# Optimization experiments

Hardware: AMD Instinct MI355X
Metric: run time of the kernel (lower is better)

The kernel has to match this reference:

```python
import jax, jax.numpy as jnp
import numpy as np

T, D, H = 2048, 256, 256
DISCOUNT = 0.99
LAMBDA = 0.9
CONT_ALPHA = 0.01


def setup_inputs() -> dict:
    key = jax.random.key(0)
    ks = jax.random.split(key, 5)
    xs = jax.random.normal(ks[0], (T, D), jnp.float32)
    gs = jax.random.normal(ks[1], (T,), jnp.float32)            # returns / targets
    dones = (jax.random.uniform(ks[2], (T,)) < 0.02).astype(jnp.float32)  # sparse episode ends
    ys = jnp.stack([gs, dones], axis=1)                          # [T, 2] as in train_step
    W1 = jax.random.normal(ks[3], (D, H), jnp.float32) * (1.0 / float(np.sqrt(D)))
    b1 = jnp.zeros((H,), jnp.float32)
    W2 = jax.random.normal(ks[4], (H, 1), jnp.float32) * (1.0 / float(np.sqrt(H)))
    b2 = jnp.zeros((1,), jnp.float32)
    return {"xs": xs, "ys": ys, "W1": W1, "b1": b1, "W2": W2, "b2": b2}


def _value(params, x):
    # Value network: self(x)[0] for a batch of 1 -> scalar prediction.
    W1, b1, W2, b2 = params
    h = jax.nn.relu(x @ W1 + b1)          # [H]
    return (h @ W2 + b2)[0]               # scalar us


def _td_lambda(xs, ys, W1, b1, W2, b2):
    params = (W1, b1, W2, b2)
    gs, dones = ys[:, 0], ys[:, 1]
    zeros = tuple(jnp.zeros_like(p) for p in params)
    val_grad = jax.value_and_grad(_value)

    def step(carry, inp):
        z, total, r = carry
        x, g, done = inp
        us, grads = val_grad(params, x)   # grads of the PREDICTION us, as in tape.gradient(us, vars)
        error = (g - us) ** 2             # compiled_loss (MSE) on a single sample
        sigma = error - r                 # continuing TD error
        r = r + CONT_ALPHA * sigma
        # eligibility trace update and accumulated update
        z = tuple(DISCOUNT * LAMBDA * zi + gi for zi, gi in zip(z, grads))
        total = tuple(ti - sigma * zi for ti, zi in zip(total, z))
        # episode reset: zero traces and average-reward estimate when done
        keep = 1.0 - (done > 0.5).astype(jnp.float32)
        z = tuple(zi * keep for zi in z)
        r = r * keep
        return (z, total, r), sigma

    init = (zeros, zeros, jnp.float32(0.0))
    (_, total, _), sigmas = jax.lax.scan(step, init, (xs, gs, dones))
    # accumulated gradients for all trainable vars (flattened) + final sigma (reported loss)
    return jnp.concatenate([t.ravel() for t in total] + [sigmas[-1][None]])


def reference(xs, ys, W1, b1, W2, b2):
    return _td_lambda(xs, ys, W1, b1, W2, b2)
```

## Files before the change

kernel.cpp:

```cpp
#include <hip/hip_runtime.h>

#define GL  0.891f
#define OMA 0.99f
#define AL  0.01f

#define OFF_H   0
#define OFF_U   524288
#define OFF_PW1 526336
#define OFF_PB1 788480
#define OFF_PW2 789504
#define WS_FLOATS 790528

__global__ __launch_bounds__(1024, 4) void fwd_kernel(
    const float* __restrict__ xs, const float* __restrict__ W1,
    const float* __restrict__ b1, const float* __restrict__ W2,
    const float* __restrict__ b2,
    float* __restrict__ Hbuf, float* __restrict__ u) {
  const int tid = threadIdx.x;
  const int j2 = tid & 127;
  const int kq = tid >> 7;
  const int kb = kq * 32;
  const int r0 = blockIdx.x * 8;
  __shared__ __align__(16) float xsl[8 * 260];
  __shared__ __align__(16) float part[8 * 2048];

  if (tid < 512) {
    const int row = tid >> 6;
    const int q4 = tid & 63;
    *reinterpret_cast<float4*>(&xsl[row * 260 + 4 * q4]) =
        *reinterpret_cast<const float4*>(&xs[(r0 + row) * 256 + 4 * q4]);
  }

  float wcur[16], wnxt[16];
#pragma unroll
  for (int kk = 0; kk < 8; ++kk) {
    wcur[2 * kk + 0] = W1[(kb + kk) * 256 + j2];
    wcur[2 * kk + 1] = W1[(kb + kk) * 256 + j2 + 128];
  }
  __syncthreads();

  float acc[16];
#pragma unroll
  for (int m = 0; m < 16; ++m) acc[m] = 0.f;
#pragma unroll
  for (int b = 0; b < 4; ++b) {
    if (b < 3) {
#pragma unroll
      for (int kk = 0; kk < 8; ++kk) {
        wnxt[2 * kk + 0] = W1[(kb + (b + 1) * 8 + kk) * 256 + j2];
        wnxt[2 * kk + 1] = W1[(kb + (b + 1) * 8 + kk) * 256 + j2 + 128];
      }
    }
    const int k = kb + b * 8;
#pragma unroll
    for (int r = 0; r < 8; ++r) {
      const float4 x0 = *reinterpret_cast<const float4*>(&xsl[r * 260 + k]);
      const float4 x1 = *reinterpret_cast<const float4*>(&xsl[r * 260 + k + 4]);
      float a0 = acc[r * 2 + 0], a1 = acc[r * 2 + 1];
      a0 = fmaf(x0.x, wcur[0], a0);  a1 = fmaf(x0.x, wcur[1], a1);
      a0 = fmaf(x0.y, wcur[2], a0);  a1 = fmaf(x0.y, wcur[3], a1);
      a0 = fmaf(x0.z, wcur[4], a0);  a1 = fmaf(x0.z, wcur[5], a1);
      a0 = fmaf(x0.w, wcur[6], a0);  a1 = fmaf(x0.w, wcur[7], a1);
      a0 = fmaf(x1.x, wcur[8], a0);  a1 = fmaf(x1.x, wcur[9], a1);
      a0 = fmaf(x1.y, wcur[10], a0); a1 = fmaf(x1.y, wcur[11], a1);
      a0 = fmaf(x1.z, wcur[12], a0); a1 = fmaf(x1.z, wcur[13], a1);
      a0 = fmaf(x1.w, wcur[14], a0); a1 = fmaf(x1.w, wcur[15], a1);
      acc[r * 2 + 0] = a0; acc[r * 2 + 1] = a1;
    }
#pragma unroll
    for (int m = 0; m < 16; ++m) wcur[m] = wnxt[m];
  }

#pragma unroll
  for (int r = 0; r < 8; ++r) {
    part[kq * 2048 + r * 256 + j2] = acc[r * 2 + 0];
    part[kq * 2048 + r * 256 + j2 + 128] = acc[r * 2 + 1];
  }
  __syncthreads();
#pragma unroll
  for (int q = 0; q < 2; ++q) {
    const int s = tid + q * 1024;
    const int j = s & 255;
    float a = b1[j];
#pragma unroll
    for (int kk = 0; kk < 8; ++kk) a += part[kk * 2048 + s];
    const float h = fmaxf(a, 0.f);
    Hbuf[r0 * 256 + s] = h;
    part[s] = h * W2[j];
  }
  __syncthreads();
  {
    const int r = tid >> 7;
    const int jj = tid & 127;
    part[r * 256 + jj] += part[r * 256 + jj + 128];
    __syncthreads();
    if (jj < 64) {
      float v = part[r * 256 + jj] + part[r * 256 + jj + 64];
#pragma unroll
      for (int s = 32; s >= 1; s >>= 1) v += __shfl_xor(v, s, 64);
      if (jj == 0) u[r0 + r] = v + b2[0];
    }
  }
}

__global__ __launch_bounds__(512, 4) void scan_w1_kernel(
    const float* __restrict__ u, const float* __restrict__ ys,
    const float* __restrict__ xs, const float* __restrict__ Hbuf,
    const float* __restrict__ W2,
    float* __restrict__ pW1, float* __restrict__ pB1, float* __restrict__ pW2,
    float* __restrict__ outp) {
  const int tid = threadIdx.x;
  const int blk = blockIdx.x;
  const int tq = blk & 3;
  const int tile = blk >> 2;
  const int dcb = tile >> 3;
  const int jc = tile & 7;
  const int d0 = dcb * 16;
  const int j0 = jc * 32;
  const int tb = tq * 512;
  const int lane = tid & 63;
  const int w = tid >> 6;
  const int jq = lane & 7;
  const int dh = (lane >> 3) & 3;
  const int tt2 = lane >> 5;
  const int tloc = w * 64 + tt2 * 32;
  const int jcol = j0 + 4 * jq;

  __shared__ __align__(16) float xt[512 * 20];
  __shared__ __align__(16) float c_l[512];
  __shared__ __align__(16) float red[8 * 576];
  __shared__ float aggA[8], aggB[8], ag2A[8], ag2B[8], wsum[8];

  const float* Hp = Hbuf + jcol;
  float4 hc[8], hn[8];
#pragma unroll
  for (int i = 0; i < 8; ++i)
    hc[i] = *reinterpret_cast<const float4*>(Hp + (tb + tloc + i) * 256);

#pragma unroll
  for (int q = 0; q < 4; ++q) {
    const int idx = tid + q * 512;
    const int row = idx >> 2;
    const int qd = idx & 3;
    *reinterpret_cast<float4*>(&xt[row * 20 + 4 * qd]) =
        *reinterpret_cast<const float4*>(&xs[(tb + row) * 256 + d0 + 4 * qd]);
  }

  float e[4], kp[4];
  {
    const float4 u4 = ((const float4*)u)[tid];
    const float uu[4] = {u4.x, u4.y, u4.z, u4.w};
#pragma unroll
    for (int q = 0; q < 2; ++q) {
      const float4 y = ((const float4*)ys)[2 * tid + q];
      const float da = y.x - uu[2 * q];
      const float db = y.z - uu[2 * q + 1];
      e[2 * q] = da * da;
      e[2 * q + 1] = db * db;
      kp[2 * q] = (y.y > 0.5f) ? 0.f : 1.f;
      kp[2 * q + 1] = (y.w > 0.5f) ? 0.f : 1.f;
    }
  }
  float A = 1.f, B = 0.f;
#pragma unroll
  for (int i = 0; i < 4; ++i) {
    const float a = kp[i] * OMA;
    B = fmaf(a, B, kp[i] * (AL * e[i]));
    A *= a;
  }
#pragma unroll
  for (int s = 1; s < 64; s <<= 1) {
    const float pA = __shfl_up(A, s, 64);
    const float pB = __shfl_up(B, s, 64);
    if (lane >= s) { B = fmaf(A, pB, B); A *= pA; }
  }
  if (lane == 63) { aggA[w] = A; aggB[w] = B; }
  __syncthreads();
  float rin;
  {
    float rw = 0.f;
    for (int v = 0; v < w; ++v) rw = fmaf(aggA[v], rw, aggB[v]);
    float lA = __shfl_up(A, 1, 64);
    float lB = __shfl_up(B, 1, 64);
    if (lane == 0) { lA = 1.f; lB = 0.f; }
    rin = fmaf(lA, rw, lB);
  }
  float sig[4];
  {
    float r = rin;
#pragma unroll
    for (int i = 0; i < 4; ++i) {
      sig[i] = e[i] - r;
      const float a = kp[i] * OMA;
      r = fmaf(a, r, kp[i] * (AL * e[i]));
    }
  }
  if (blk == 0 && tid == 511) outp[66049] = sig[3];

  float A2 = 1.f, B2 = 0.f;
#pragma unroll
  for (int i = 3; i >= 0; --i) {
    const float a = GL * kp[i];
    B2 = fmaf(a, B2, -sig[i]);
    A2 *= a;
  }
#pragma unroll
  for (int s = 1; s < 64; s <<= 1) {
    const float nA = __shfl_down(A2, s, 64);
    const float nB = __shfl_down(B2, s, 64);
    if (lane + s < 64) { B2 = fmaf(A2, nB, B2); A2 *= nA; }
  }
  if (lane == 0) { ag2A[w] = A2; ag2B[w] = B2; }
  __syncthreads();
  float cin;
  {
    float cw = 0.f;
    for (int v = 7; v > w; --v) cw = fmaf(ag2A[v], cw, ag2B[v]);
    float lA = __shfl_down(A2, 1, 64);
    float lB = __shfl_down(B2, 1, 64);
    if (lane == 63) { lA = 1.f; lB = 0.f; }
    cin = fmaf(lA, cw, lB);
  }
  float cr[4];
  float cc = cin, csum = 0.f;
#pragma unroll
  for (int i = 3; i >= 0; --i) {
    cc = fmaf(GL * kp[i], cc, -sig[i]);
    cr[i] = cc;
    csum += cc;
  }
  if ((tid >> 7) == tq) {
    const int bl = 4 * (tid - tq * 128);
    *reinterpret_cast<float4*>(&c_l[bl]) = make_float4(cr[0], cr[1], cr[2], cr[3]);
  }
  if (blk == 0) {
#pragma unroll
    for (int s = 32; s >= 1; s >>= 1) csum += __shfl_xor(csum, s, 64);
    if (lane == 0) wsum[w] = csum;
  }
  __syncthreads();
  if (blk == 0 && tid == 0) {
    float s = 0.f;
#pragma unroll
    for (int v = 0; v < 8; ++v) s += wsum[v];
    outp[66048] = s;
  }

  const float4 w24 = *reinterpret_cast<const float4*>(W2 + jcol);
  float acc[16];
#pragma unroll
  for (int m = 0; m < 16; ++m) acc[m] = 0.f;
  float sb[4] = {0.f, 0.f, 0.f, 0.f}, sw[4] = {0.f, 0.f, 0.f, 0.f};
  const bool do_bw = (dcb == 0);

#pragma unroll
  for (int b = 0; b < 4; ++b) {
    if (b < 3) {
#pragma unroll
      for (int i = 0; i < 8; ++i)
        hn[i] = *reinterpret_cast<const float4*>(
            Hp + (tb + tloc + (b + 1) * 8 + i) * 256);
    }
#pragma unroll
    for (int i = 0; i < 8; ++i) {
      const int row = tloc + b * 8 + i;
      const float ct = c_l[row];
      const float4 h = hc[i];
      const float gc0 = (h.x > 0.f) ? w24.x * ct : 0.f;
      const float gc1 = (h.y > 0.f) ? w24.y * ct : 0.f;
      const float gc2 = (h.z > 0.f) ? w24.z * ct : 0.f;
      const float gc3 = (h.w > 0.f) ? w24.w * ct : 0.f;
      if (do_bw) {
        sb[0] += gc0; sb[1] += gc1; sb[2] += gc2; sb[3] += gc3;
        sw[0] = fmaf(ct, h.x, sw[0]); sw[1] = fmaf(ct, h.y, sw[1]);
        sw[2] = fmaf(ct, h.z, sw[2]); sw[3] = fmaf(ct, h.w, sw[3]);
      }
      const float4 xv = *reinterpret_cast<const float4*>(&xt[row * 20 + dh * 4]);
      acc[0]  = fmaf(gc0, xv.x, acc[0]);
      acc[1]  = fmaf(gc1, xv.x, acc[1]);
      acc[2]  = fmaf(gc2, xv.x, acc[2]);
      acc[3]  = fmaf(gc3, xv.x, acc[3]);
      acc[4]  = fmaf(gc0, xv.y, acc[4]);
      acc[5]  = fmaf(gc1, xv.y, acc[5]);
      acc[6]  = fmaf(gc2, xv.y, acc[6]);
      acc[7]  = fmaf(gc3, xv.y, acc[7]);
      acc[8]  = fmaf(gc0, xv.z, acc[8]);
      acc[9]  = fmaf(gc1, xv.z, acc[9]);
      acc[10] = fmaf(gc2, xv.z, acc[10]);
      acc[11] = fmaf(gc3, xv.z, acc[11]);
      acc[12] = fmaf(gc0, xv.w, acc[12]);
      acc[13] = fmaf(gc1, xv.w, acc[13]);
      acc[14] = fmaf(gc2, xv.w, acc[14]);
      acc[15] = fmaf(gc3, xv.w, acc[15]);
    }
#pragma unroll
    for (int i = 0; i < 8; ++i) hc[i] = hn[i];
  }

#pragma unroll
  for (int m = 0; m < 16; ++m) acc[m] += __shfl_xor(acc[m], 32, 64);
  if (do_bw) {
#pragma unroll
    for (int c = 0; c < 4; ++c) {
      sb[c] += __shfl_xor(sb[c], 8, 64);
      sb[c] += __shfl_xor(sb[c], 16, 64);
      sb[c] += __shfl_xor(sb[c], 32, 64);
      sw[c] += __shfl_xor(sw[c], 8, 64);
      sw[c] += __shfl_xor(sw[c], 16, 64);
      sw[c] += __shfl_xor(sw[c], 32, 64);
    }
  }
  if (lane < 32) {
#pragma unroll
    for (int x = 0; x < 4; ++x)
      *reinterpret_cast<float4*>(&red[w * 576 + (dh * 4 + x) * 32 + jq * 4]) =
          make_float4(acc[x * 4 + 0], acc[x * 4 + 1], acc[x * 4 + 2], acc[x * 4 + 3]);
  }
  if (do_bw && lane < 8) {
    *reinterpret_cast<float4*>(&red[w * 576 + 16 * 32 + lane * 4]) =
        make_float4(0.25f * sb[0], 0.25f * sb[1], 0.25f * sb[2], 0.25f * sb[3]);
    *reinterpret_cast<float4*>(&red[w * 576 + 17 * 32 + lane * 4]) =
        make_float4(0.25f * sw[0], 0.25f * sw[1], 0.25f * sw[2], 0.25f * sw[3]);
  }
  __syncthreads();
  {
    const int col = tid & 31;
    const int dd = tid >> 5;
    float s = 0.f;
#pragma unroll
    for (int v = 0; v < 8; ++v) s += red[v * 576 + dd * 32 + col];
    pW1[tq * 65536 + (d0 + dd) * 256 + j0 + col] = s;
  }
  if (do_bw && tid < 64) {
    const int col = tid & 31;
    const int sel = tid >> 5;
    float s = 0.f;
#pragma unroll
    for (int v = 0; v < 8; ++v) s += red[v * 576 + (16 + sel) * 32 + col];
    (sel ? pW2 : pB1)[tq * 256 + j0 + col] = s;
  }
}

__global__ __launch_bounds__(256) void reduce_kernel(
    const float* __restrict__ pW1, const float* __restrict__ pB1,
    const float* __restrict__ pW2, float* __restrict__ outp) {
  if (blockIdx.x < 64) {
    const int i0 = blockIdx.x * 1024 + threadIdx.x * 4;
    float4 s = make_float4(0.f, 0.f, 0.f, 0.f);
#pragma unroll
    for (int q = 0; q < 4; ++q) {
      const float4 v = *reinterpret_cast<const float4*>(pW1 + q * 65536 + i0);
      s.x += v.x; s.y += v.y; s.z += v.z; s.w += v.w;
    }
    *reinterpret_cast<float4*>(outp + i0) = s;
  } else {
    const int j = threadIdx.x;
    float sb = 0.f, sw = 0.f;
#pragma unroll
    for (int q = 0; q < 4; ++q) {
      sb += pB1[q * 256 + j];
      sw += pW2[q * 256 + j];
    }
    outp[65536 + j] = sb;
    outp[65792 + j] = sw;
  }
}

extern "C" void kernel_launch(void* const* d_in, const int* in_sizes, int n_in,
                              void* d_out, int out_size, void* d_ws, size_t ws_size,
                              hipStream_t stream) {
  const float* xs = (const float*)d_in[0];
  const float* ys = (const float*)d_in[1];
  const float* W1 = (const float*)d_in[2];
  const float* b1 = (const float*)d_in[3];
  const float* W2 = (const float*)d_in[4];
  const float* b2 = (const float*)d_in[5];
  float* outp = (float*)d_out;
  float* ws = (float*)d_ws;

  if (ws_size < (size_t)WS_FLOATS * sizeof(float)) return;

  float* Hbuf = ws + OFF_H;
  float* ubuf = ws + OFF_U;
  float* pW1  = ws + OFF_PW1;
  float* pB1  = ws + OFF_PB1;
  float* pW2  = ws + OFF_PW2;

  fwd_kernel<<<256, 1024, 0, stream>>>(xs, W1, b1, W2, b2, Hbuf, ubuf);
  scan_w1_kernel<<<512, 512, 0, stream>>>(ubuf, ys, xs, Hbuf, W2,
                                          pW1, pB1, pW2, outp);
  reduce_kernel<<<65, 256, 0, stream>>>(pW1, pB1, pW2, outp);
}
```

Before: 26.88 us.

## Drop time-split partials and reduce kernel; each block covers all timesteps

The scan/W1-gradient kernel no longer splits the time axis into four quarters that write partial sums reduced by a third kernel. Each block now owns a smaller 8x16 (d,j) tile across all 2048 timesteps and writes final results directly to the output. xs is streamed from global memory into registers with double buffering instead of being staged in shared memory. This removes one kernel launch and the partial-buffer round trip. In exchange each block runs a longer serial loop and does more cross-lane shuffle reductions.

```diff
diff --git a/kernel.cpp b/kernel.cpp
--- a/kernel.cpp
+++ b/kernel.cpp
@@ -4,12 +4,9 @@
 #define OMA 0.99f
 #define AL  0.01f
 
-#define OFF_H   0
-#define OFF_U   524288
-#define OFF_PW1 526336
-#define OFF_PB1 788480
-#define OFF_PW2 789504
-#define WS_FLOATS 790528
+#define OFF_H 0
+#define OFF_U 524288
+#define WS_FLOATS 526336
 
 __global__ __launch_bounds__(1024, 4) void fwd_kernel(
     const float* __restrict__ xs, const float* __restrict__ W1,
@@ -106,44 +103,33 @@
 __global__ __launch_bounds__(512, 4) void scan_w1_kernel(
     const float* __restrict__ u, const float* __restrict__ ys,
     const float* __restrict__ xs, const float* __restrict__ Hbuf,
-    const float* __restrict__ W2,
-    float* __restrict__ pW1, float* __restrict__ pB1, float* __restrict__ pW2,
-    float* __restrict__ outp) {
+    const float* __restrict__ W2, float* __restrict__ outp) {
   const int tid = threadIdx.x;
   const int blk = blockIdx.x;
-  const int tq = blk & 3;
-  const int tile = blk >> 2;
-  const int dcb = tile >> 3;
-  const int jc = tile & 7;
-  const int d0 = dcb * 16;
-  const int j0 = jc * 32;
-  const int tb = tq * 512;
+  const int dcb = blk >> 4;
+  const int jc = blk & 15;
+  const int d0 = dcb * 8;
+  const int j0 = jc * 16;
   const int lane = tid & 63;
   const int w = tid >> 6;
-  const int jq = lane & 7;
-  const int dh = (lane >> 3) & 3;
-  const int tt2 = lane >> 5;
-  const int tloc = w * 64 + tt2 * 32;
+  const int jq = lane & 3;
+  const int dh = (lane >> 2) & 1;
+  const int tt2 = lane >> 3;
+  const int tbase = w * 64 + tt2 * 8;
   const int jcol = j0 + 4 * jq;
-
-  __shared__ __align__(16) float xt[512 * 20];
-  __shared__ __align__(16) float c_l[512];
-  __shared__ __align__(16) float red[8 * 576];
+  const int dcol = d0 + 4 * dh;
+
+  __shared__ __align__(16) float c_l[2048];
+  __shared__ __align__(16) float red[1280];
   __shared__ float aggA[8], aggB[8], ag2A[8], ag2B[8], wsum[8];
 
   const float* Hp = Hbuf + jcol;
-  float4 hc[8], hn[8];
-#pragma unroll
-  for (int i = 0; i < 8; ++i)
-    hc[i] = *reinterpret_cast<const float4*>(Hp + (tb + tloc + i) * 256);
-
-#pragma unroll
-  for (int q = 0; q < 4; ++q) {
-    const int idx = tid + q * 512;
-    const int row = idx >> 2;
-    const int qd = idx & 3;
-    *reinterpret_cast<float4*>(&xt[row * 20 + 4 * qd]) =
-        *reinterpret_cast<const float4*>(&xs[(tb + row) * 256 + d0 + 4 * qd]);
+  const float* Xp = xs + dcol;
+  float4 hc[4], hn[4], xc[4], xn[4];
+#pragma unroll
+  for (int i = 0; i < 4; ++i) {
+    hc[i] = *reinterpret_cast<const float4*>(Hp + (tbase + i) * 256);
+    xc[i] = *reinterpret_cast<const float4*>(Xp + (tbase + i) * 256);
   }
 
   float e[4], kp[4];
@@ -229,10 +215,7 @@
     cr[i] = cc;
     csum += cc;
   }
-  if ((tid >> 7) == tq) {
-    const int bl = 4 * (tid - tq * 128);
-    *reinterpret_cast<float4*>(&c_l[bl]) = make_float4(cr[0], cr[1], cr[2], cr[3]);
-  }
+  *reinterpret_cast<float4*>(&c_l[4 * tid]) = make_float4(cr[0], cr[1], cr[2], cr[3]);
   if (blk == 0) {
 #pragma unroll
     for (int s = 32; s >= 1; s >>= 1) csum += __shfl_xor(csum, s, 64);
@@ -253,19 +236,22 @@
   float sb[4] = {0.f, 0.f, 0.f, 0.f}, sw[4] = {0.f, 0.f, 0.f, 0.f};
   const bool do_bw = (dcb == 0);
 
-#pragma unroll
-  for (int b = 0; b < 4; ++b) {
-    if (b < 3) {
-#pragma unroll
-      for (int i = 0; i < 8; ++i)
-        hn[i] = *reinterpret_cast<const float4*>(
-            Hp + (tb + tloc + (b + 1) * 8 + i) * 256);
-    }
-#pragma unroll
-    for (int i = 0; i < 8; ++i) {
-      const int row = tloc + b * 8 + i;
-      const float ct = c_l[row];
+#pragma unroll 1
+  for (int r8 = 0; r8 < 8; ++r8) {
+    const int tcur = (r8 >> 1) * 512 + tbase + (r8 & 1) * 4;
+    if (r8 < 7) {
+      const int tnx = ((r8 + 1) >> 1) * 512 + tbase + ((r8 + 1) & 1) * 4;
+#pragma unroll
+      for (int i = 0; i < 4; ++i) {
+        hn[i] = *reinterpret_cast<const float4*>(Hp + (tnx + i) * 256);
+        xn[i] = *reinterpret_cast<const float4*>(Xp + (tnx + i) * 256);
+      }
+    }
+#pragma unroll
+    for (int i = 0; i < 4; ++i) {
+      const float ct = c_l[tcur + i];
       const float4 h = hc[i];
+      const float4 xv = xc[i];
       const float gc0 = (h.x > 0.f) ? w24.x * ct : 0.f;
       const float gc1 = (h.y > 0.f) ? w24.y * ct : 0.f;
       const float gc2 = (h.z > 0.f) ? w24.z * ct : 0.f;
@@ -275,7 +261,6 @@
         sw[0] = fmaf(ct, h.x, sw[0]); sw[1] = fmaf(ct, h.y, sw[1]);
         sw[2] = fmaf(ct, h.z, sw[2]); sw[3] = fmaf(ct, h.w, sw[3]);
       }
-      const float4 xv = *reinterpret_cast<const float4*>(&xt[row * 20 + dh * 4]);
       acc[0]  = fmaf(gc0, xv.x, acc[0]);
       acc[1]  = fmaf(gc1, xv.x, acc[1]);
       acc[2]  = fmaf(gc2, xv.x, acc[2]);
@@ -294,75 +279,56 @@
       acc[15] = fmaf(gc3, xv.w, acc[15]);
     }
 #pragma unroll
-    for (int i = 0; i < 8; ++i) hc[i] = hn[i];
-  }
-
-#pragma unroll
-  for (int m = 0; m < 16; ++m) acc[m] += __shfl_xor(acc[m], 32, 64);
+    for (int i = 0; i < 4; ++i) { hc[i] = hn[i]; xc[i] = xn[i]; }
+  }
+
+#pragma unroll
+  for (int m = 0; m < 16; ++m) {
+    acc[m] += __shfl_xor(acc[m], 8, 64);
+    acc[m] += __shfl_xor(acc[m], 16, 64);
+    acc[m] += __shfl_xor(acc[m], 32, 64);
+  }
   if (do_bw) {
 #pragma unroll
-    for (int c = 0; c < 4; ++c) {
-      sb[c] += __shfl_xor(sb[c], 8, 64);
-      sb[c] += __shfl_xor(sb[c], 16, 64);
-      sb[c] += __shfl_xor(sb[c], 32, 64);
-      sw[c] += __shfl_xor(sw[c], 8, 64);
-      sw[c] += __shfl_xor(sw[c], 16, 64);
-      sw[c] += __shfl_xor(sw[c], 32, 64);
-    }
-  }
-  if (lane < 32) {
+    for (int q = 0; q < 4; ++q) {
+      sb[q] += __shfl_xor(sb[q], 4, 64);
+      sb[q] += __shfl_xor(sb[q], 8, 64);
+      sb[q] += __shfl_xor(sb[q], 16, 64);
+      sb[q] += __shfl_xor(sb[q], 32, 64);
+      sw[q] += __shfl_xor(sw[q], 4, 64);
+      sw[q] += __shfl_xor(sw[q], 8, 64);
+      sw[q] += __shfl_xor(sw[q], 16, 64);
+      sw[q] += __shfl_xor(sw[q], 32, 64);
+    }
+  }
+  if (lane < 8) {
 #pragma unroll
     for (int x = 0; x < 4; ++x)
-      *reinterpret_cast<float4*>(&red[w * 576 + (dh * 4 + x) * 32 + jq * 4]) =
+      *reinterpret_cast<float4*>(&red[w * 160 + (dh * 4 + x) * 16 + jq * 4]) =
           make_float4(acc[x * 4 + 0], acc[x * 4 + 1], acc[x * 4 + 2], acc[x * 4 + 3]);
   }
-  if (do_bw && lane < 8) {
-    *reinterpret_cast<float4*>(&red[w * 576 + 16 * 32 + lane * 4]) =
-        make_float4(0.25f * sb[0], 0.25f * sb[1], 0.25f * sb[2], 0.25f * sb[3]);
-    *reinterpret_cast<float4*>(&red[w * 576 + 17 * 32 + lane * 4]) =
-        make_float4(0.25f * sw[0], 0.25f * sw[1], 0.25f * sw[2], 0.25f * sw[3]);
-  }
-  __syncthreads();
-  {
-    const int col = tid & 31;
-    const int dd = tid >> 5;
+  if (do_bw && lane < 4) {
+    *reinterpret_cast<float4*>(&red[w * 160 + 128 + lane * 4]) =
+        make_float4(0.5f * sb[0], 0.5f * sb[1], 0.5f * sb[2], 0.5f * sb[3]);
+    *reinterpret_cast<float4*>(&red[w * 160 + 144 + lane * 4]) =
+        make_float4(0.5f * sw[0], 0.5f * sw[1], 0.5f * sw[2], 0.5f * sw[3]);
+  }
+  __syncthreads();
+  if (tid < 128) {
+    const int od = tid >> 4;
+    const int oj = tid & 15;
     float s = 0.f;
 #pragma unroll
-    for (int v = 0; v < 8; ++v) s += red[v * 576 + dd * 32 + col];
-    pW1[tq * 65536 + (d0 + dd) * 256 + j0 + col] = s;
-  }
-  if (do_bw && tid < 64) {
-    const int col = tid & 31;
-    const int sel = tid >> 5;
+    for (int v = 0; v < 8; ++v) s += red[v * 160 + od * 16 + oj];
+    outp[(d0 + od) * 256 + j0 + oj] = s;
+  } else if (do_bw && tid < 160) {
+    const int q = tid - 128;
+    const int col = q & 15;
+    const int sel = q >> 4;
     float s = 0.f;
 #pragma unroll
-    for (int v = 0; v < 8; ++v) s += red[v * 576 + (16 + sel) * 32 + col];
-    (sel ? pW2 : pB1)[tq * 256 + j0 + col] = s;
-  }
-}
-
-__global__ __launch_bounds__(256) void reduce_kernel(
-    const float* __restrict__ pW1, const float* __restrict__ pB1,
-    const float* __restrict__ pW2, float* __restrict__ outp) {
-  if (blockIdx.x < 64) {
-    const int i0 = blockIdx.x * 1024 + threadIdx.x * 4;
-    float4 s = make_float4(0.f, 0.f, 0.f, 0.f);
-#pragma unroll
-    for (int q = 0; q < 4; ++q) {
-      const float4 v = *reinterpret_cast<const float4*>(pW1 + q * 65536 + i0);
-      s.x += v.x; s.y += v.y; s.z += v.z; s.w += v.w;
-    }
-    *reinterpret_cast<float4*>(outp + i0) = s;
-  } else {
-    const int j = threadIdx.x;
-    float sb = 0.f, sw = 0.f;
-#pragma unroll
-    for (int q = 0; q < 4; ++q) {
-      sb += pB1[q * 256 + j];
-      sw += pW2[q * 256 + j];
-    }
-    outp[65536 + j] = sb;
-    outp[65792 + j] = sw;
+    for (int v = 0; v < 8; ++v) s += red[v * 160 + 128 + sel * 16 + col];
+    outp[(sel ? 65792 : 65536) + j0 + col] = s;
   }
 }
 
@@ -382,12 +348,7 @@
 
   float* Hbuf = ws + OFF_H;
   float* ubuf = ws + OFF_U;
-  float* pW1  = ws + OFF_PW1;
-  float* pB1  = ws + OFF_PB1;
-  float* pW2  = ws + OFF_PW2;
 
   fwd_kernel<<<256, 1024, 0, stream>>>(xs, W1, b1, W2, b2, Hbuf, ubuf);
-  scan_w1_kernel<<<512, 512, 0, stream>>>(ubuf, ys, xs, Hbuf, W2,
-                                          pW1, pB1, pW2, outp);
-  reduce_kernel<<<65, 256, 0, stream>>>(pW1, pB1, pW2, outp);
+  scan_w1_kernel<<<512, 512, 0, stream>>>(ubuf, ys, xs, Hbuf, W2, outp);
 }
```

Result: slower. 32.42 us (+20.6%).
